# Optimization experiments

Measured on AMD Instinct MI355X. Metric: run time of the kernel, lower is better.

## Reference

```python
import jax, jax.numpy as jnp
import numpy as np

K = 3            # attn_kernels
PAD = K // 2
NORM_SCALE = 1.0
EPS = 1e-4


def _conv(x, w, pad):
    # NCHW conv, stride 1, symmetric padding
    return jax.lax.conv_general_dilated(
        x, w, window_strides=(1, 1), padding=[(pad, pad), (pad, pad)],
        dimension_numbers=('NCHW', 'OIHW', 'NCHW'))


def _unfold(x, k, stride, pad):
    # torch.nn.functional.unfold: returns [B, C*k*k, L], feature order (c, kh, kw),
    # L in row-major patch order.
    if pad:
        x = jnp.pad(x, ((0, 0), (0, 0), (pad, pad), (pad, pad)))
    B, C, H, W = x.shape
    oh = (H - k) // stride + 1
    ow = (W - k) // stride + 1
    cols = []
    for i in range(k):          # small fixed k*k loop (k=3)
        for j in range(k):
            cols.append(x[:, :, i:i + stride * (oh - 1) + 1:stride,
                               j:j + stride * (ow - 1) + 1:stride])
    p = jnp.stack(cols, axis=2)             # [B, C, k*k, oh, ow]
    return p.reshape(B, C * k * k, oh * ow)


def setup_inputs() -> dict:
    key = jax.random.key(0)
    k1, k2, k3, k4 = jax.random.split(key, 4)
    B, Cin, Cout, H, W = 8, 192, 192, 96, 96
    fan = Cin * K * K
    x1 = jax.random.normal(k1, (B, Cin, H, W), jnp.float32)
    x2 = jax.random.normal(k2, (B, Cin, H, W), jnp.float32)
    key_w = jax.random.normal(k3, (Cin, Cin, K, K), jnp.float32) / np.sqrt(fan)
    query_w = jax.random.normal(k4, (Cout, Cin, K, K), jnp.float32) / np.sqrt(fan)
    kernel_momentum = jnp.zeros((), jnp.float32)  # init 0.0 as in module
    return {"x1": x1, "x2": x2, "key_w": key_w, "query_w": query_w,
            "kernel_momentum": kernel_momentum}


def reference(x1, x2, key_w, query_w, kernel_momentum):
    B, Cin, H, W = x1.shape
    Cout = query_w.shape[0]
    fk = K * K

    # key: conv then non-overlapping unfold -> [B, fk, Cin, L]
    kf = _unfold(_conv(x1, key_w, PAD), K, stride=K, pad=0)
    L = kf.shape[-1]
    kf = kf.reshape(B, Cin, fk, L).transpose(0, 2, 1, 3)      # [B, fk, Cin, L]

    # query: conv then non-overlapping unfold -> [B, fk, L, Cout]
    qf = _unfold(_conv(x2, query_w, PAD), K, stride=K, pad=0)
    qf = qf.reshape(B, Cout, fk, L).transpose(0, 2, 3, 1)     # [B, fk, L, Cout]

    # attention kernels: [B, fk, Cin, Cout] -> [B, Cout, Cin*fk]
    attn = jnp.einsum('bkcl,bklo->bkco', kf, qf)
    attn = attn.transpose(0, 3, 2, 1).reshape(B, Cout, Cin * fk)

    # custom global mean/std normalization with momentum (torch std is unbiased)
    m = attn.mean()
    s = jnp.std(attn, ddof=1)
    attn = kernel_momentum * attn + NORM_SCALE * (attn - m) / (s + EPS)

    # apply kernels to dense (stride-1, padded) unfold of x1
    v = _unfold(x1, K, stride=1, pad=PAD)                     # [B, Cin*fk, H*W]
    out = jnp.einsum('bcf,bfl->bcl', attn, v)                 # [B, Cout, H*W]
    return out.reshape(B, Cout, H, W)
```

## Files before the change

### kernel.cpp

```cpp
#include <hip/hip_runtime.h>
#include <math.h>

typedef __attribute__((ext_vector_type(8))) short s16x8;
typedef __attribute__((ext_vector_type(4))) short s16x4;
typedef __attribute__((ext_vector_type(4))) float f32x4;

typedef unsigned int u32;
typedef __attribute__((address_space(3))) u32* lds_u32p;
typedef const __attribute__((address_space(1))) u32* glb_u32p;

namespace {

constexpr int B  = 8;
constexpr int C  = 192;
constexpr int H  = 96;
constexpr int W  = 96;
constexpr int FK = 9;
constexpr int HP = 98;
constexpr int L  = 1024;
constexpr int WCHUNK = FK * 12 * 6;
constexpr int WELEM  = WCHUNK * 512;
constexpr size_t XPAD_ELEMS = (size_t)B * HP * HP * 192;

__device__ inline unsigned short f2b(float f) {
    unsigned int x = __float_as_uint(f);
    x += 0x7fffu + ((x >> 16) & 1u);
    return (unsigned short)(x >> 16);
}

__global__ __launch_bounds__(256) void border_zero(unsigned short* __restrict__ xpad) {
    const int c   = blockIdx.x * 256 + threadIdx.x;
    const int c16 = c % 24;
    const int p_  = c / 24;
    const int pos = p_ % 388;
    const int bt  = p_ / 388;
    int yy, xx;
    if (pos < 98)       { yy = 0;          xx = pos; }
    else if (pos < 196) { yy = 97;         xx = pos - 98; }
    else if (pos < 292) { yy = pos - 195;  xx = 0; }
    else                { yy = pos - 291;  xx = 97; }
    const size_t off = (((size_t)bt * HP + yy) * HP + xx) * 192 + c16 * 8;
    *(s16x8*)(xpad + off) = (s16x8){0, 0, 0, 0, 0, 0, 0, 0};
}

__global__ __launch_bounds__(256) void prep_x(const float* __restrict__ x1,
                                              const float* __restrict__ x2,
                                              unsigned short* __restrict__ xpadT) {
    __shared__ float xs[192][33];
    const int tid = threadIdx.x;
    const int x0  = blockIdx.x * 32;
    const int y   = blockIdx.y;
    const int zz  = blockIdx.z;
    const int b   = zz & 7, t = zz >> 3;
    const float* x = t ? x2 : x1;
    unsigned short* dst = xpadT + (size_t)t * XPAD_ELEMS;
    for (int e = tid; e < 192 * 32; e += 256) {
        const int ci = e >> 5, xx = e & 31;
        xs[ci][xx] = x[(((size_t)b * C + ci) * H + y) * W + x0 + xx];
    }
    __syncthreads();
    for (int e = tid; e < 32 * 192; e += 256) {
        const int pos = e / 192, ci = e - pos * 192;
        dst[(((size_t)(b * HP + y + 1)) * HP + x0 + pos + 1) * 192 + ci] = f2b(xs[ci][pos]);
    }
}

__global__ __launch_bounds__(256) void prep_w(const float* __restrict__ kw,
                                              const float* __restrict__ qw,
                                              unsigned short* __restrict__ kwA,
                                              unsigned short* __restrict__ qwA) {
    int idx = blockIdx.x * 256 + threadIdx.x;
    const float* src = kw;
    unsigned short* dst = kwA;
    if (idx >= WELEM) { idx -= WELEM; src = qw; dst = qwA; }
    const int chunk = idx >> 9, within = idx & 511;
    const int lane = within >> 3, t = within & 7;
    const int kg = lane >> 4, r15 = lane & 15;
    const int cc = chunk % 6, c2 = chunk / 6;
    const int cot = c2 % 12, p = c2 / 12;
    const int co = cot * 16 + r15;
    const int ci = cc * 32 + kg * 8 + t;
    dst[idx] = f2b(src[((size_t)co * C + ci) * FK + p]);
}

template <bool OUTF32, bool PERB, bool DUAL>
__global__ __launch_bounds__(256, 3)
void conv_mfma(const unsigned short* __restrict__ xpadA,
               const unsigned short* __restrict__ xpadB,
               const unsigned short* __restrict__ wA,
               const unsigned short* __restrict__ wB,
               void* __restrict__ youtA,
               void* __restrict__ youtB) {
    __shared__ __align__(16) char smem[2][19200];
    const int tid  = threadIdx.x;
    const int y    = blockIdx.x;
    const int sx   = blockIdx.y;
    const int zz   = blockIdx.z;
    const int b    = DUAL ? (zz & 7) : zz;
    const int t    = DUAL ? (zz >> 3) : 0;
    const unsigned short* xpadT = (DUAL && t) ? xpadB : xpadA;
    const unsigned short* wbase = (DUAL && t) ? wB : wA;
    void* yout = (DUAL && t) ? youtB : youtA;
    const int lane = tid & 63, wc = tid >> 6;
    const int ln15 = lane & 15, kg = lane >> 4;

    const unsigned short* wp = PERB ? (wbase + (size_t)b * WELEM) : wbase;

    int gfull[4];
#pragma unroll
    for (int it = 0; it < 4; ++it) {
        const int m = it * 256 + tid;
        const int q = m / 24, c16 = m - q * 24;
        gfull[it] = (sx * 48 + q) * 384 + ((c16 * 16) ^ ((q & 7) << 4));
    }
    int gtail = 0;
    if (tid < 176) {
        const int m = 1024 + tid;
        const int q = m / 24, c16 = m - q * 24;
        gtail = (sx * 48 + q) * 384 + ((c16 * 16) ^ ((q & 7) << 4));
    }

    auto stage = [&](char* lb, int prow) {
        const char* rowbase = (const char*)(xpadT + ((size_t)(b * HP + prow)) * HP * 192);
#pragma unroll
        for (int it = 0; it < 4; ++it)
            __builtin_amdgcn_global_load_lds(
                (glb_u32p)(const void*)(rowbase + gfull[it]),
                (lds_u32p)(void*)(lb + it * 4096 + wc * 1024), 16, 0, 0);
        if (tid < 176)
            __builtin_amdgcn_global_load_lds(
                (glb_u32p)(const void*)(rowbase + gtail),
                (lds_u32p)(void*)(lb + 16384 + wc * 1024), 16, 0, 0);
    };

    f32x4 acc[3][3];
#pragma unroll
    for (int i = 0; i < 3; ++i)
#pragma unroll
        for (int j = 0; j < 3; ++j)
            acc[i][j] = (f32x4){0.f, 0.f, 0.f, 0.f};

    stage(smem[0], y);

    for (int dy = 0; dy < 3; ++dy) {
        asm volatile("s_waitcnt vmcnt(0)" ::: "memory");
        __syncthreads();
        const char* lb = smem[dy & 1];

#pragma unroll
        for (int cc = 0; cc < 6; ++cc) {
            s16x8 af[3][3];
#pragma unroll
            for (int dx = 0; dx < 3; ++dx)
#pragma unroll
                for (int i = 0; i < 3; ++i) {
                    const int chunkid = ((3 * dy + dx) * 12 + wc * 3 + i) * 6 + cc;
                    af[dx][i] = *(const s16x8*)(wp + (size_t)chunkid * 512 + lane * 8);
                }
            if (cc == 5) {
                __builtin_amdgcn_sched_barrier(0);
                if (dy < 2) stage((char*)smem[(dy + 1) & 1], y + dy + 1);
                __builtin_amdgcn_sched_barrier(0);
            }
            s16x8 bv[3][3];
#pragma unroll
            for (int j = 0; j < 3; ++j)
#pragma unroll
                for (int dx = 0; dx < 3; ++dx) {
                    const int q = j * 16 + ln15 + dx;
                    bv[j][dx] = *(const s16x8*)(lb + q * 384 +
                                    ((cc * 64 + kg * 16) ^ ((q & 7) << 4)));
                }
#pragma unroll
            for (int i = 0; i < 3; ++i)
#pragma unroll
                for (int j = 0; j < 3; ++j)
#pragma unroll
                    for (int dx = 0; dx < 3; ++dx)
                        acc[i][j] = __builtin_amdgcn_mfma_f32_16x16x32_bf16(
                            af[dx][i], bv[j][dx], acc[i][j], 0, 0, 0);
        }
    }

    if (!OUTF32) {
        unsigned short* yb = (unsigned short*)yout;
        const int ph = y % 3, lh = y / 3;
        int poff[3];
#pragma unroll
        for (int j = 0; j < 3; ++j) {
            const int s  = sx * 48 + j * 16 + ln15;
            const int pw = s % 3, lw = s / 3;
            poff[j] = ((b * FK + ph * 3 + pw) * C) * L + lh * 32 + lw;
        }
#pragma unroll
        for (int i = 0; i < 3; ++i)
#pragma unroll
            for (int rr = 0; rr < 4; ++rr) {
                const int co = wc * 48 + i * 16 + kg * 4 + rr;
#pragma unroll
                for (int j = 0; j < 3; ++j)
                    yb[(size_t)poff[j] + co * L] = f2b(acc[i][j][rr]);
            }
    } else {
        float* yf = (float*)yout;
#pragma unroll
        for (int i = 0; i < 3; ++i)
#pragma unroll
            for (int rr = 0; rr < 4; ++rr) {
                const int co = wc * 48 + i * 16 + kg * 4 + rr;
                const size_t base = (((size_t)b * C + co) * H + y) * W;
#pragma unroll
                for (int j = 0; j < 3; ++j)
                    yf[base + sx * 48 + j * 16 + ln15] = acc[i][j][rr];
            }
    }
}

__global__ __launch_bounds__(256, 3)
void attn_mfma(const unsigned short* __restrict__ kcS,
               const unsigned short* __restrict__ qcS,
               float* __restrict__ attnT,
               double* __restrict__ part) {
    __shared__ __align__(16) char smem[2][24576];
    const int tid  = threadIdx.x;
    const int lane = tid & 63, wid = tid >> 6;
    const int wq   = wid & 1, wp = wid >> 1;
    const int ln15 = lane & 15, kg = lane >> 4;
    const int of   = blockIdx.x & 1, cf = blockIdx.x >> 1;
    const int p    = blockIdx.y, b = blockIdx.z;

    const char* Abase = (const char*)(kcS + ((size_t)(b * FK + p) * C + cf * 96) * L);
    const char* Bbase = (const char*)(qcS + ((size_t)(b * FK + p) * C + of * 96) * L);

    int gofs[3];
#pragma unroll
    for (int it = 0; it < 3; ++it) {
        const int chunk = it * 256 + tid;
        const int row = chunk >> 3, c16 = chunk & 7;
        gofs[it] = row * 2048 + ((c16 * 16) ^ ((row & 7) << 4));
    }

    auto stage = [&](int bufi, int t) {
        const char* Ab = Abase + t * 128;
        const char* Bb = Bbase + t * 128;
        char* lb = (char*)smem[bufi];
#pragma unroll
        for (int it = 0; it < 3; ++it)
            __builtin_amdgcn_global_load_lds(
                (glb_u32p)(const void*)(Ab + gofs[it]),
                (lds_u32p)(void*)(lb + it * 4096 + wid * 1024), 16, 0, 0);
#pragma unroll
        for (int it = 0; it < 3; ++it)
            __builtin_amdgcn_global_load_lds(
                (glb_u32p)(const void*)(Bb + gofs[it]),
                (lds_u32p)(void*)(lb + 12288 + it * 4096 + wid * 1024), 16, 0, 0);
    };

    f32x4 acc[3][3];
#pragma unroll
    for (int i = 0; i < 3; ++i)
#pragma unroll
        for (int j = 0; j < 3; ++j)
            acc[i][j] = (f32x4){0.f, 0.f, 0.f, 0.f};

    stage(0, 0);
    asm volatile("s_waitcnt vmcnt(0)" ::: "memory");
    __syncthreads();

    for (int t = 0; t < 16; ++t) {
        if (t < 15) stage((t + 1) & 1, t + 1);
        const char* lb = (const char*)smem[t & 1];
#pragma unroll
        for (int ks = 0; ks < 2; ++ks) {
            s16x8 af[3], bf[3];
#pragma unroll
            for (int i = 0; i < 3; ++i) {
                const int row = wp * 48 + i * 16 + ln15;
                af[i] = *(const s16x8*)(lb + row * 128 +
                                        ((ks * 64 + kg * 16) ^ ((row & 7) << 4)));
            }
#pragma unroll
            for (int j = 0; j < 3; ++j) {
                const int row = wq * 48 + j * 16 + ln15;
                bf[j] = *(const s16x8*)(lb + 12288 + row * 128 +
                                        ((ks * 64 + kg * 16) ^ ((row & 7) << 4)));
            }
#pragma unroll
            for (int i = 0; i < 3; ++i)
#pragma unroll
                for (int j = 0; j < 3; ++j)
                    acc[i][j] = __builtin_amdgcn_mfma_f32_16x16x32_bf16(
                        af[i], bf[j], acc[i][j], 0, 0, 0);
        }
        if (t < 15) {
            asm volatile("s_waitcnt vmcnt(0)" ::: "memory");
            __syncthreads();
        }
    }

    __syncthreads();
    double s = 0.0, ss = 0.0;
#pragma unroll
    for (int i = 0; i < 3; ++i)
#pragma unroll
        for (int j = 0; j < 3; ++j)
#pragma unroll
            for (int r = 0; r < 4; ++r) {
                const double v = (double)acc[i][j][r];
                s += v; ss += v * v;
            }
    double* ls  = (double*)&smem[0][0];
    double* lss = ls + 256;
    ls[tid] = s; lss[tid] = ss;
    __syncthreads();
    for (int st = 128; st; st >>= 1) {
        if (tid < st) { ls[tid] += ls[tid + st]; lss[tid] += lss[tid + st]; }
        __syncthreads();
    }
    if (tid == 0) {
        const int bf_ = ((b * FK + p) << 2) + blockIdx.x;
        part[2 * bf_]     = ls[0];
        part[2 * bf_ + 1] = lss[0];
    }

    float* ap = attnT + (size_t)(b * FK + p) * C * C;
#pragma unroll
    for (int i = 0; i < 3; ++i) {
        const int c0 = cf * 96 + wp * 48 + i * 16 + kg * 4;
#pragma unroll
        for (int j = 0; j < 3; ++j) {
            const int o = of * 96 + wq * 48 + j * 16 + ln15;
            *(f32x4*)(ap + o * C + c0) = acc[i][j];
        }
    }
}

__global__ __launch_bounds__(256) void finalize_k(const double* __restrict__ part,
                                                  const float* __restrict__ momp,
                                                  float* __restrict__ scal) {
    __shared__ double ls[256], lss[256];
    double s = 0.0, ss = 0.0;
    for (int i = threadIdx.x; i < 288; i += 256) {
        s += part[2 * i]; ss += part[2 * i + 1];
    }
    ls[threadIdx.x] = s; lss[threadIdx.x] = ss;
    __syncthreads();
    for (int st = 128; st; st >>= 1) {
        if (threadIdx.x < st) {
            ls[threadIdx.x]  += ls[threadIdx.x + st];
            lss[threadIdx.x] += lss[threadIdx.x + st];
        }
        __syncthreads();
    }
    if (threadIdx.x == 0) {
        const double n    = (double)(B * FK * C * C);
        const double mean = ls[0] / n;
        double var        = (lss[0] - ls[0] * ls[0] / n) / (n - 1.0);
        if (var < 0.0) var = 0.0;
        const double scale = 1.0 / (sqrt(var) + 1e-4);
        scal[0] = (float)((double)momp[0] + scale);
        scal[1] = (float)(-mean * scale);
    }
}

__global__ __launch_bounds__(256) void norm_w(const float* __restrict__ attnT,
                                              const float* __restrict__ scal,
                                              unsigned short* __restrict__ o) {
    const float alpha = scal[0], beta = scal[1];
    const int g = (blockIdx.x * 256 + threadIdx.x) * 4;
    const int chunk = g >> 9, within = g & 511;
    const int lane = within >> 3, t0 = within & 7;
    const int cc = chunk % 6, c2 = chunk / 6;
    const int cot = c2 % 12, pb = c2 / 12;
    const int p = pb % FK, b = pb / FK;
    const int co = cot * 16 + (lane & 15);
    const int ci = cc * 32 + (lane >> 4) * 8 + t0;
    const float4 v = *(const float4*)(attnT + (((size_t)(b * FK + p) * C + co) * C + ci));
    s16x4 r;
    r[0] = (short)f2b(fmaf(alpha, v.x, beta));
    r[1] = (short)f2b(fmaf(alpha, v.y, beta));
    r[2] = (short)f2b(fmaf(alpha, v.z, beta));
    r[3] = (short)f2b(fmaf(alpha, v.w, beta));
    *(s16x4*)(o + g) = r;
}

}

extern "C" void kernel_launch(void* const* d_in, const int* in_sizes, int n_in,
                              void* d_out, int out_size, void* d_ws, size_t ws_size,
                              hipStream_t stream) {
    (void)in_sizes; (void)n_in; (void)out_size; (void)ws_size;
    const float* x1   = (const float*)d_in[0];
    const float* x2   = (const float*)d_in[1];
    const float* kw   = (const float*)d_in[2];
    const float* qw   = (const float*)d_in[3];
    const float* momp = (const float*)d_in[4];

    char* ws = (char*)d_ws;
    unsigned short* xpad1 = (unsigned short*)ws;
    unsigned short* xpad2 = (unsigned short*)(ws + 29503488);
    unsigned short* kwA   = (unsigned short*)(ws + 59006976);
    unsigned short* qwA   = (unsigned short*)(ws + 59670528);
    unsigned short* kcS   = (unsigned short*)(ws + 60334080);
    float*          attnT = (float*)(ws + 88645632);
    double*         part  = (double*)(ws + 99262464);
    float*          scal  = (float*)(ws + 99278848);
    unsigned short* normW = kcS;
    unsigned short* qcS   = (unsigned short*)d_out;

    border_zero<<<582, 256, 0, stream>>>(xpad1);

    prep_x<<<dim3(3, 96, 16), 256, 0, stream>>>(x1, x2, xpad1);
    prep_w<<<2592, 256, 0, stream>>>(kw, qw, kwA, qwA);

    conv_mfma<false, false, true><<<dim3(96, 2, 16), 256, 0, stream>>>(
        xpad1, xpad2, kwA, qwA, kcS, qcS);

    attn_mfma<<<dim3(4, 9, 8), 256, 0, stream>>>(kcS, qcS, attnT, part);
    finalize_k<<<1, 256, 0, stream>>>(part, momp, scal);

    norm_w<<<2592, 256, 0, stream>>>(attnT, scal, normW);
    conv_mfma<true, true, false><<<dim3(96, 2, 8), 256, 0, stream>>>(
        xpad1, nullptr, normW, nullptr, (float*)d_out, nullptr);
}
```

Before: 265.3 us.

## Compute two output rows per conv block to reuse weight fragments

Each conv block now produces two output rows instead of one. It loads all four needed padded input rows into LDS up front, and every weight fragment read from global memory feeds MFMAs for both rows, which halves weight traffic per output. The cost is the loss of the double-buffered staging overlap. LDS use grows to about 77KB and the accumulators double, so launch bounds drop to 2 blocks per SM and the grid is halved.

```diff
diff --git a/kernel.cpp b/kernel.cpp
--- a/kernel.cpp
+++ b/kernel.cpp
@@ -84,16 +84,16 @@
 }
 
 template <bool OUTF32, bool PERB, bool DUAL>
-__global__ __launch_bounds__(256, 3)
+__global__ __launch_bounds__(256, 2)
 void conv_mfma(const unsigned short* __restrict__ xpadA,
                const unsigned short* __restrict__ xpadB,
                const unsigned short* __restrict__ wA,
                const unsigned short* __restrict__ wB,
                void* __restrict__ youtA,
                void* __restrict__ youtB) {
-    __shared__ __align__(16) char smem[2][19200];
+    __shared__ __align__(16) char smem[4 * 50 * 384];
     const int tid  = threadIdx.x;
-    const int y    = blockIdx.x;
+    const int y0   = blockIdx.x * 2;
     const int sx   = blockIdx.y;
     const int zz   = blockIdx.z;
     const int b    = DUAL ? (zz & 7) : zz;
@@ -106,47 +106,37 @@
 
     const unsigned short* wp = PERB ? (wbase + (size_t)b * WELEM) : wbase;
 
-    int gfull[4];
-#pragma unroll
-    for (int it = 0; it < 4; ++it) {
-        const int m = it * 256 + tid;
-        const int q = m / 24, c16 = m - q * 24;
-        gfull[it] = (sx * 48 + q) * 384 + ((c16 * 16) ^ ((q & 7) << 4));
-    }
-    int gtail = 0;
-    if (tid < 176) {
-        const int m = 1024 + tid;
-        const int q = m / 24, c16 = m - q * 24;
-        gtail = (sx * 48 + q) * 384 + ((c16 * 16) ^ ((q & 7) << 4));
-    }
-
-    auto stage = [&](char* lb, int prow) {
-        const char* rowbase = (const char*)(xpadT + ((size_t)(b * HP + prow)) * HP * 192);
-#pragma unroll
-        for (int it = 0; it < 4; ++it)
-            __builtin_amdgcn_global_load_lds(
-                (glb_u32p)(const void*)(rowbase + gfull[it]),
-                (lds_u32p)(void*)(lb + it * 4096 + wc * 1024), 16, 0, 0);
-        if (tid < 176)
-            __builtin_amdgcn_global_load_lds(
-                (glb_u32p)(const void*)(rowbase + gtail),
-                (lds_u32p)(void*)(lb + 16384 + wc * 1024), 16, 0, 0);
-    };
-
-    f32x4 acc[3][3];
-#pragma unroll
-    for (int i = 0; i < 3; ++i)
-#pragma unroll
-        for (int j = 0; j < 3; ++j)
-            acc[i][j] = (f32x4){0.f, 0.f, 0.f, 0.f};
-
-    stage(smem[0], y);
-
+    {
+        const char* base = (const char*)(xpadT + ((size_t)(b * HP + y0)) * HP * 192);
+#pragma unroll
+        for (int it = 0; it < 19; ++it) {
+            const int m = it * 256 + tid;
+            if (it < 18 || tid < 192) {
+                const int r  = m / 1200, rm = m - r * 1200;
+                const int p  = rm / 24,  c16 = rm - p * 24;
+                const int go = r * 37632 + (sx * 48 + p) * 384 +
+                               ((c16 * 16) ^ ((p & 7) << 4));
+                __builtin_amdgcn_global_load_lds(
+                    (glb_u32p)(const void*)(base + go),
+                    (lds_u32p)(void*)(smem + it * 4096 + wc * 1024), 16, 0, 0);
+            }
+        }
+    }
+
+    f32x4 acc[2][3][3];
+#pragma unroll
+    for (int yy = 0; yy < 2; ++yy)
+#pragma unroll
+        for (int i = 0; i < 3; ++i)
+#pragma unroll
+            for (int j = 0; j < 3; ++j)
+                acc[yy][i][j] = (f32x4){0.f, 0.f, 0.f, 0.f};
+
+    asm volatile("s_waitcnt vmcnt(0)" ::: "memory");
+    __syncthreads();
+
+#pragma unroll
     for (int dy = 0; dy < 3; ++dy) {
-        asm volatile("s_waitcnt vmcnt(0)" ::: "memory");
-        __syncthreads();
-        const char* lb = smem[dy & 1];
-
 #pragma unroll
         for (int cc = 0; cc < 6; ++cc) {
             s16x8 af[3][3];
@@ -157,62 +147,65 @@
                     const int chunkid = ((3 * dy + dx) * 12 + wc * 3 + i) * 6 + cc;
                     af[dx][i] = *(const s16x8*)(wp + (size_t)chunkid * 512 + lane * 8);
                 }
-            if (cc == 5) {
-                __builtin_amdgcn_sched_barrier(0);
-                if (dy < 2) stage((char*)smem[(dy + 1) & 1], y + dy + 1);
-                __builtin_amdgcn_sched_barrier(0);
-            }
-            s16x8 bv[3][3];
-#pragma unroll
-            for (int j = 0; j < 3; ++j)
-#pragma unroll
-                for (int dx = 0; dx < 3; ++dx) {
-                    const int q = j * 16 + ln15 + dx;
-                    bv[j][dx] = *(const s16x8*)(lb + q * 384 +
-                                    ((cc * 64 + kg * 16) ^ ((q & 7) << 4)));
+#pragma unroll
+            for (int yy = 0; yy < 2; ++yy) {
+                const int rr = yy + dy;
+                s16x8 bv[3][3];
+#pragma unroll
+                for (int j = 0; j < 3; ++j)
+#pragma unroll
+                    for (int dx = 0; dx < 3; ++dx) {
+                        const int q = j * 16 + ln15 + dx;
+                        bv[j][dx] = *(const s16x8*)(smem + (rr * 50 + q) * 384 +
+                                        ((cc * 64 + kg * 16) ^ ((q & 7) << 4)));
+                    }
+#pragma unroll
+                for (int i = 0; i < 3; ++i)
+#pragma unroll
+                    for (int j = 0; j < 3; ++j)
+#pragma unroll
+                        for (int dx = 0; dx < 3; ++dx)
+                            acc[yy][i][j] = __builtin_amdgcn_mfma_f32_16x16x32_bf16(
+                                af[dx][i], bv[j][dx], acc[yy][i][j], 0, 0, 0);
+            }
+        }
+    }
+
+#pragma unroll
+    for (int yy = 0; yy < 2; ++yy) {
+        const int y = y0 + yy;
+        if (!OUTF32) {
+            unsigned short* yb = (unsigned short*)yout;
+            const int ph = y % 3, lh = y / 3;
+            int poff[3];
+#pragma unroll
+            for (int j = 0; j < 3; ++j) {
+                const int s  = sx * 48 + j * 16 + ln15;
+                const int pw = s % 3, lw = s / 3;
+                poff[j] = ((b * FK + ph * 3 + pw) * C) * L + lh * 32 + lw;
+            }
+#pragma unroll
+            for (int i = 0; i < 3; ++i)
+#pragma unroll
+                for (int rr = 0; rr < 4; ++rr) {
+                    const int co = wc * 48 + i * 16 + kg * 4 + rr;
+#pragma unroll
+                    for (int j = 0; j < 3; ++j)
+                        yb[(size_t)poff[j] + co * L] = f2b(acc[yy][i][j][rr]);
                 }
+        } else {
+            float* yf = (float*)yout;
 #pragma unroll
             for (int i = 0; i < 3; ++i)
 #pragma unroll
-                for (int j = 0; j < 3; ++j)
-#pragma unroll
-                    for (int dx = 0; dx < 3; ++dx)
-                        acc[i][j] = __builtin_amdgcn_mfma_f32_16x16x32_bf16(
-                            af[dx][i], bv[j][dx], acc[i][j], 0, 0, 0);
-        }
-    }
-
-    if (!OUTF32) {
-        unsigned short* yb = (unsigned short*)yout;
-        const int ph = y % 3, lh = y / 3;
-        int poff[3];
-#pragma unroll
-        for (int j = 0; j < 3; ++j) {
-            const int s  = sx * 48 + j * 16 + ln15;
-            const int pw = s % 3, lw = s / 3;
-            poff[j] = ((b * FK + ph * 3 + pw) * C) * L + lh * 32 + lw;
-        }
-#pragma unroll
-        for (int i = 0; i < 3; ++i)
-#pragma unroll
-            for (int rr = 0; rr < 4; ++rr) {
-                const int co = wc * 48 + i * 16 + kg * 4 + rr;
-#pragma unroll
-                for (int j = 0; j < 3; ++j)
-                    yb[(size_t)poff[j] + co * L] = f2b(acc[i][j][rr]);
-            }
-    } else {
-        float* yf = (float*)yout;
-#pragma unroll
-        for (int i = 0; i < 3; ++i)
-#pragma unroll
-            for (int rr = 0; rr < 4; ++rr) {
-                const int co = wc * 48 + i * 16 + kg * 4 + rr;
-                const size_t base = (((size_t)b * C + co) * H + y) * W;
-#pragma unroll
-                for (int j = 0; j < 3; ++j)
-                    yf[base + sx * 48 + j * 16 + ln15] = acc[i][j][rr];
-            }
+                for (int rr = 0; rr < 4; ++rr) {
+                    const int co = wc * 48 + i * 16 + kg * 4 + rr;
+                    const size_t base = (((size_t)b * C + co) * H + y) * W;
+#pragma unroll
+                    for (int j = 0; j < 3; ++j)
+                        yf[base + sx * 48 + j * 16 + ln15] = acc[yy][i][j][rr];
+                }
+        }
     }
 }
 
@@ -413,13 +406,13 @@
     prep_x<<<dim3(3, 96, 16), 256, 0, stream>>>(x1, x2, xpad1);
     prep_w<<<2592, 256, 0, stream>>>(kw, qw, kwA, qwA);
 
-    conv_mfma<false, false, true><<<dim3(96, 2, 16), 256, 0, stream>>>(
+    conv_mfma<false, false, true><<<dim3(48, 2, 16), 256, 0, stream>>>(
         xpad1, xpad2, kwA, qwA, kcS, qcS);
 
     attn_mfma<<<dim3(4, 9, 8), 256, 0, stream>>>(kcS, qcS, attnT, part);
     finalize_k<<<1, 256, 0, stream>>>(part, momp, scal);
 
     norm_w<<<2592, 256, 0, stream>>>(attnT, scal, normW);
-    conv_mfma<true, true, false><<<dim3(96, 2, 8), 256, 0, stream>>>(
+    conv_mfma<true, true, false><<<dim3(48, 2, 8), 256, 0, stream>>>(
         xpad1, nullptr, normW, nullptr, (float*)d_out, nullptr);
 }
```

Result: slower. 556.9 us (+109.9%).

## Widen conv tiles to full output rows and drop LDS double buffering

Applied to the files above, without the earlier changes.

The conv kernel now computes a full 96-pixel output row per block instead of two 48-pixel halves. This halves the grid and reuses each weight fragment load across six column tiles instead of three, cutting redundant weight traffic. The double-buffered LDS staging is replaced by a single full-row buffer loaded after a barrier, so the next row's global-to-LDS load no longer overlaps compute. Fewer blocks, more accumulator registers and no occupancy hint may reduce latency hiding.

```diff
diff --git a/kernel.cpp b/kernel.cpp
--- a/kernel.cpp
+++ b/kernel.cpp
@@ -84,18 +84,17 @@
 }
 
 template <bool OUTF32, bool PERB, bool DUAL>
-__global__ __launch_bounds__(256, 3)
+__global__ __launch_bounds__(256)
 void conv_mfma(const unsigned short* __restrict__ xpadA,
                const unsigned short* __restrict__ xpadB,
                const unsigned short* __restrict__ wA,
                const unsigned short* __restrict__ wB,
                void* __restrict__ youtA,
                void* __restrict__ youtB) {
-    __shared__ __align__(16) char smem[2][19200];
+    __shared__ __align__(16) char smem[HP * 384];
     const int tid  = threadIdx.x;
     const int y    = blockIdx.x;
-    const int sx   = blockIdx.y;
-    const int zz   = blockIdx.z;
+    const int zz   = blockIdx.y;
     const int b    = DUAL ? (zz & 7) : zz;
     const int t    = DUAL ? (zz >> 3) : 0;
     const unsigned short* xpadT = (DUAL && t) ? xpadB : xpadA;
@@ -106,89 +105,79 @@
 
     const unsigned short* wp = PERB ? (wbase + (size_t)b * WELEM) : wbase;
 
-    int gfull[4];
-#pragma unroll
-    for (int it = 0; it < 4; ++it) {
+    int gofs[9];
+#pragma unroll
+    for (int it = 0; it < 9; ++it) {
         const int m = it * 256 + tid;
         const int q = m / 24, c16 = m - q * 24;
-        gfull[it] = (sx * 48 + q) * 384 + ((c16 * 16) ^ ((q & 7) << 4));
+        gofs[it] = q * 384 + ((c16 * 16) ^ ((q & 7) << 4));
     }
     int gtail = 0;
-    if (tid < 176) {
-        const int m = 1024 + tid;
+    if (tid < 48) {
+        const int m = 2304 + tid;
         const int q = m / 24, c16 = m - q * 24;
-        gtail = (sx * 48 + q) * 384 + ((c16 * 16) ^ ((q & 7) << 4));
-    }
-
-    auto stage = [&](char* lb, int prow) {
-        const char* rowbase = (const char*)(xpadT + ((size_t)(b * HP + prow)) * HP * 192);
-#pragma unroll
-        for (int it = 0; it < 4; ++it)
+        gtail = q * 384 + ((c16 * 16) ^ ((q & 7) << 4));
+    }
+
+    auto stage = [&](int prow) {
+        const char* rb = (const char*)(xpadT + ((size_t)(b * HP + prow)) * HP * 192);
+#pragma unroll
+        for (int it = 0; it < 9; ++it)
             __builtin_amdgcn_global_load_lds(
-                (glb_u32p)(const void*)(rowbase + gfull[it]),
-                (lds_u32p)(void*)(lb + it * 4096 + wc * 1024), 16, 0, 0);
-        if (tid < 176)
+                (glb_u32p)(const void*)(rb + gofs[it]),
+                (lds_u32p)(void*)(smem + it * 4096 + wc * 1024), 16, 0, 0);
+        if (tid < 48)
             __builtin_amdgcn_global_load_lds(
-                (glb_u32p)(const void*)(rowbase + gtail),
-                (lds_u32p)(void*)(lb + 16384 + wc * 1024), 16, 0, 0);
+                (glb_u32p)(const void*)(rb + gtail),
+                (lds_u32p)(void*)(smem + 36864 + wc * 1024), 16, 0, 0);
     };
 
-    f32x4 acc[3][3];
+    f32x4 acc[3][6];
 #pragma unroll
     for (int i = 0; i < 3; ++i)
 #pragma unroll
-        for (int j = 0; j < 3; ++j)
+        for (int j = 0; j < 6; ++j)
             acc[i][j] = (f32x4){0.f, 0.f, 0.f, 0.f};
 
-    stage(smem[0], y);
-
+    stage(y);
+
+#pragma unroll 1
     for (int dy = 0; dy < 3; ++dy) {
         asm volatile("s_waitcnt vmcnt(0)" ::: "memory");
         __syncthreads();
-        const char* lb = smem[dy & 1];
-
-#pragma unroll
+
+#pragma unroll 1
         for (int cc = 0; cc < 6; ++cc) {
-            s16x8 af[3][3];
-#pragma unroll
-            for (int dx = 0; dx < 3; ++dx)
-#pragma unroll
-                for (int i = 0; i < 3; ++i) {
-                    const int chunkid = ((3 * dy + dx) * 12 + wc * 3 + i) * 6 + cc;
-                    af[dx][i] = *(const s16x8*)(wp + (size_t)chunkid * 512 + lane * 8);
+#pragma unroll
+            for (int dx = 0; dx < 3; ++dx) {
+                const int cid = (((3 * dy + dx) * 12 + wc * 3) * 6 + cc);
+                const s16x8 af0 = *(const s16x8*)(wp + (size_t)cid * 512 + lane * 8);
+                const s16x8 af1 = *(const s16x8*)(wp + (size_t)(cid + 6) * 512 + lane * 8);
+                const s16x8 af2 = *(const s16x8*)(wp + (size_t)(cid + 12) * 512 + lane * 8);
+#pragma unroll
+                for (int j = 0; j < 6; ++j) {
+                    const int q = j * 16 + ln15 + dx;
+                    const s16x8 bv = *(const s16x8*)(smem + q * 384 +
+                                        ((cc * 64 + kg * 16) ^ ((q & 7) << 4)));
+                    acc[0][j] = __builtin_amdgcn_mfma_f32_16x16x32_bf16(af0, bv, acc[0][j], 0, 0, 0);
+                    acc[1][j] = __builtin_amdgcn_mfma_f32_16x16x32_bf16(af1, bv, acc[1][j], 0, 0, 0);
+                    acc[2][j] = __builtin_amdgcn_mfma_f32_16x16x32_bf16(af2, bv, acc[2][j], 0, 0, 0);
                 }
-            if (cc == 5) {
-                __builtin_amdgcn_sched_barrier(0);
-                if (dy < 2) stage((char*)smem[(dy + 1) & 1], y + dy + 1);
-                __builtin_amdgcn_sched_barrier(0);
-            }
-            s16x8 bv[3][3];
-#pragma unroll
-            for (int j = 0; j < 3; ++j)
-#pragma unroll
-                for (int dx = 0; dx < 3; ++dx) {
-                    const int q = j * 16 + ln15 + dx;
-                    bv[j][dx] = *(const s16x8*)(lb + q * 384 +
-                                    ((cc * 64 + kg * 16) ^ ((q & 7) << 4)));
-                }
-#pragma unroll
-            for (int i = 0; i < 3; ++i)
-#pragma unroll
-                for (int j = 0; j < 3; ++j)
-#pragma unroll
-                    for (int dx = 0; dx < 3; ++dx)
-                        acc[i][j] = __builtin_amdgcn_mfma_f32_16x16x32_bf16(
-                            af[dx][i], bv[j][dx], acc[i][j], 0, 0, 0);
+            }
+        }
+        if (dy < 2) {
+            __syncthreads();
+            stage(y + dy + 1);
         }
     }
 
     if (!OUTF32) {
         unsigned short* yb = (unsigned short*)yout;
         const int ph = y % 3, lh = y / 3;
-        int poff[3];
-#pragma unroll
-        for (int j = 0; j < 3; ++j) {
-            const int s  = sx * 48 + j * 16 + ln15;
+        int poff[6];
+#pragma unroll
+        for (int j = 0; j < 6; ++j) {
+            const int s  = j * 16 + ln15;
             const int pw = s % 3, lw = s / 3;
             poff[j] = ((b * FK + ph * 3 + pw) * C) * L + lh * 32 + lw;
         }
@@ -198,7 +187,7 @@
             for (int rr = 0; rr < 4; ++rr) {
                 const int co = wc * 48 + i * 16 + kg * 4 + rr;
 #pragma unroll
-                for (int j = 0; j < 3; ++j)
+                for (int j = 0; j < 6; ++j)
                     yb[(size_t)poff[j] + co * L] = f2b(acc[i][j][rr]);
             }
     } else {
@@ -210,8 +199,8 @@
                 const int co = wc * 48 + i * 16 + kg * 4 + rr;
                 const size_t base = (((size_t)b * C + co) * H + y) * W;
 #pragma unroll
-                for (int j = 0; j < 3; ++j)
-                    yf[base + sx * 48 + j * 16 + ln15] = acc[i][j][rr];
+                for (int j = 0; j < 6; ++j)
+                    yf[base + j * 16 + ln15] = acc[i][j][rr];
             }
     }
 }
@@ -413,13 +402,13 @@
     prep_x<<<dim3(3, 96, 16), 256, 0, stream>>>(x1, x2, xpad1);
     prep_w<<<2592, 256, 0, stream>>>(kw, qw, kwA, qwA);
 
-    conv_mfma<false, false, true><<<dim3(96, 2, 16), 256, 0, stream>>>(
+    conv_mfma<false, false, true><<<dim3(96, 16), 256, 0, stream>>>(
         xpad1, xpad2, kwA, qwA, kcS, qcS);
 
     attn_mfma<<<dim3(4, 9, 8), 256, 0, stream>>>(kcS, qcS, attnT, part);
     finalize_k<<<1, 256, 0, stream>>>(part, momp, scal);
 
     norm_w<<<2592, 256, 0, stream>>>(attnT, scal, normW);
-    conv_mfma<true, true, false><<<dim3(96, 2, 8), 256, 0, stream>>>(
+    conv_mfma<true, true, false><<<dim3(96, 8), 256, 0, stream>>>(
         xpad1, nullptr, normW, nullptr, (float*)d_out, nullptr);
 }
```

Result: faster. 259.3 us (-2.3%).

## Specialize final conv to full-row tiles with per-wave weight reuse

Applied to the files above, without the earlier changes.

Splits the templated conv into a front kernel for the dual key/query convs and a new final conv kernel. The final conv kernel processes a whole 96-pixel row per block (6 column tiles instead of 3), staging the full padded row in LDS. Each weight fragment is loaded directly from global memory once and reused across six MMA column tiles, which halves weight traffic and redundant halo staging. In exchange it doubles the accumulators, drops the double-buffered LDS pipeline in favour of a single buffer with syncs, and uses a larger LDS footprint that may lower occupancy.

```diff
diff --git a/kernel.cpp b/kernel.cpp
--- a/kernel.cpp
+++ b/kernel.cpp
@@ -83,28 +83,25 @@
     dst[idx] = f2b(src[((size_t)co * C + ci) * FK + p]);
 }
 
-template <bool OUTF32, bool PERB, bool DUAL>
 __global__ __launch_bounds__(256, 3)
-void conv_mfma(const unsigned short* __restrict__ xpadA,
-               const unsigned short* __restrict__ xpadB,
-               const unsigned short* __restrict__ wA,
-               const unsigned short* __restrict__ wB,
-               void* __restrict__ youtA,
-               void* __restrict__ youtB) {
+void conv_front(const unsigned short* __restrict__ xpadA,
+                const unsigned short* __restrict__ xpadB,
+                const unsigned short* __restrict__ wA,
+                const unsigned short* __restrict__ wB,
+                void* __restrict__ youtA,
+                void* __restrict__ youtB) {
     __shared__ __align__(16) char smem[2][19200];
     const int tid  = threadIdx.x;
     const int y    = blockIdx.x;
     const int sx   = blockIdx.y;
     const int zz   = blockIdx.z;
-    const int b    = DUAL ? (zz & 7) : zz;
-    const int t    = DUAL ? (zz >> 3) : 0;
-    const unsigned short* xpadT = (DUAL && t) ? xpadB : xpadA;
-    const unsigned short* wbase = (DUAL && t) ? wB : wA;
-    void* yout = (DUAL && t) ? youtB : youtA;
+    const int b    = zz & 7;
+    const int t    = zz >> 3;
+    const unsigned short* xpadT = t ? xpadB : xpadA;
+    const unsigned short* wp    = t ? wB : wA;
+    void* yout = t ? youtB : youtA;
     const int lane = tid & 63, wc = tid >> 6;
     const int ln15 = lane & 15, kg = lane >> 4;
-
-    const unsigned short* wp = PERB ? (wbase + (size_t)b * WELEM) : wbase;
 
     int gfull[4];
 #pragma unroll
@@ -182,38 +179,115 @@
         }
     }
 
-    if (!OUTF32) {
-        unsigned short* yb = (unsigned short*)yout;
-        const int ph = y % 3, lh = y / 3;
-        int poff[3];
-#pragma unroll
-        for (int j = 0; j < 3; ++j) {
-            const int s  = sx * 48 + j * 16 + ln15;
-            const int pw = s % 3, lw = s / 3;
-            poff[j] = ((b * FK + ph * 3 + pw) * C) * L + lh * 32 + lw;
-        }
-#pragma unroll
-        for (int i = 0; i < 3; ++i)
-#pragma unroll
-            for (int rr = 0; rr < 4; ++rr) {
-                const int co = wc * 48 + i * 16 + kg * 4 + rr;
-#pragma unroll
-                for (int j = 0; j < 3; ++j)
-                    yb[(size_t)poff[j] + co * L] = f2b(acc[i][j][rr]);
+    unsigned short* yb = (unsigned short*)yout;
+    const int ph = y % 3, lh = y / 3;
+    int poff[3];
+#pragma unroll
+    for (int j = 0; j < 3; ++j) {
+        const int s  = sx * 48 + j * 16 + ln15;
+        const int pw = s % 3, lw = s / 3;
+        poff[j] = ((b * FK + ph * 3 + pw) * C) * L + lh * 32 + lw;
+    }
+#pragma unroll
+    for (int i = 0; i < 3; ++i)
+#pragma unroll
+        for (int rr = 0; rr < 4; ++rr) {
+            const int co = wc * 48 + i * 16 + kg * 4 + rr;
+#pragma unroll
+            for (int j = 0; j < 3; ++j)
+                yb[(size_t)poff[j] + co * L] = f2b(acc[i][j][rr]);
+        }
+}
+
+__global__ __launch_bounds__(256)
+void conv_final(const unsigned short* __restrict__ xpadT,
+                const unsigned short* __restrict__ wA,
+                float* __restrict__ yout) {
+    __shared__ __align__(16) char smem[HP * 384];
+    const int tid  = threadIdx.x;
+    const int y    = blockIdx.x;
+    const int b    = blockIdx.y;
+    const int lane = tid & 63, wc = tid >> 6;
+    const int ln15 = lane & 15, kg = lane >> 4;
+
+    const unsigned short* wp = wA + (size_t)b * WELEM;
+
+    int gofs[9];
+#pragma unroll
+    for (int it = 0; it < 9; ++it) {
+        const int m = it * 256 + tid;
+        const int q = m / 24, c16 = m - q * 24;
+        gofs[it] = q * 384 + ((c16 * 16) ^ ((q & 7) << 4));
+    }
+    int gtail = 0;
+    if (tid < 48) {
+        const int m = 2304 + tid;
+        const int q = m / 24, c16 = m - q * 24;
+        gtail = q * 384 + ((c16 * 16) ^ ((q & 7) << 4));
+    }
+
+    auto stage = [&](int prow) {
+        const char* rb = (const char*)(xpadT + ((size_t)(b * HP + prow)) * HP * 192);
+#pragma unroll
+        for (int it = 0; it < 9; ++it)
+            __builtin_amdgcn_global_load_lds(
+                (glb_u32p)(const void*)(rb + gofs[it]),
+                (lds_u32p)(void*)(smem + it * 4096 + wc * 1024), 16, 0, 0);
+        if (tid < 48)
+            __builtin_amdgcn_global_load_lds(
+                (glb_u32p)(const void*)(rb + gtail),
+                (lds_u32p)(void*)(smem + 36864 + wc * 1024), 16, 0, 0);
+    };
+
+    f32x4 acc[3][6];
+#pragma unroll
+    for (int i = 0; i < 3; ++i)
+#pragma unroll
+        for (int j = 0; j < 6; ++j)
+            acc[i][j] = (f32x4){0.f, 0.f, 0.f, 0.f};
+
+    stage(y);
+
+#pragma unroll 1
+    for (int dy = 0; dy < 3; ++dy) {
+        asm volatile("s_waitcnt vmcnt(0)" ::: "memory");
+        __syncthreads();
+
+#pragma unroll 1
+        for (int cc = 0; cc < 6; ++cc) {
+#pragma unroll
+            for (int dx = 0; dx < 3; ++dx) {
+                const int cid = (((3 * dy + dx) * 12 + wc * 3) * 6 + cc);
+                const s16x8 af0 = *(const s16x8*)(wp + (size_t)cid * 512 + lane * 8);
+                const s16x8 af1 = *(const s16x8*)(wp + (size_t)(cid + 6) * 512 + lane * 8);
+                const s16x8 af2 = *(const s16x8*)(wp + (size_t)(cid + 12) * 512 + lane * 8);
+#pragma unroll
+                for (int j = 0; j < 6; ++j) {
+                    const int q = j * 16 + ln15 + dx;
+                    const s16x8 bv = *(const s16x8*)(smem + q * 384 +
+                                        ((cc * 64 + kg * 16) ^ ((q & 7) << 4)));
+                    acc[0][j] = __builtin_amdgcn_mfma_f32_16x16x32_bf16(af0, bv, acc[0][j], 0, 0, 0);
+                    acc[1][j] = __builtin_amdgcn_mfma_f32_16x16x32_bf16(af1, bv, acc[1][j], 0, 0, 0);
+                    acc[2][j] = __builtin_amdgcn_mfma_f32_16x16x32_bf16(af2, bv, acc[2][j], 0, 0, 0);
+                }
             }
-    } else {
-        float* yf = (float*)yout;
-#pragma unroll
-        for (int i = 0; i < 3; ++i)
-#pragma unroll
-            for (int rr = 0; rr < 4; ++rr) {
-                const int co = wc * 48 + i * 16 + kg * 4 + rr;
-                const size_t base = (((size_t)b * C + co) * H + y) * W;
-#pragma unroll
-                for (int j = 0; j < 3; ++j)
-                    yf[base + sx * 48 + j * 16 + ln15] = acc[i][j][rr];
-            }
-    }
+        }
+        if (dy < 2) {
+            __syncthreads();
+            stage(y + dy + 1);
+        }
+    }
+
+#pragma unroll
+    for (int i = 0; i < 3; ++i)
+#pragma unroll
+        for (int rr = 0; rr < 4; ++rr) {
+            const int co = wc * 48 + i * 16 + kg * 4 + rr;
+            const size_t base = (((size_t)b * C + co) * H + y) * W;
+#pragma unroll
+            for (int j = 0; j < 6; ++j)
+                yout[base + j * 16 + ln15] = acc[i][j][rr];
+        }
 }
 
 __global__ __launch_bounds__(256, 3)
@@ -413,13 +487,12 @@
     prep_x<<<dim3(3, 96, 16), 256, 0, stream>>>(x1, x2, xpad1);
     prep_w<<<2592, 256, 0, stream>>>(kw, qw, kwA, qwA);
 
-    conv_mfma<false, false, true><<<dim3(96, 2, 16), 256, 0, stream>>>(
+    conv_front<<<dim3(96, 2, 16), 256, 0, stream>>>(
         xpad1, xpad2, kwA, qwA, kcS, qcS);
 
     attn_mfma<<<dim3(4, 9, 8), 256, 0, stream>>>(kcS, qcS, attnT, part);
     finalize_k<<<1, 256, 0, stream>>>(part, momp, scal);
 
     norm_w<<<2592, 256, 0, stream>>>(attnT, scal, normW);
-    conv_mfma<true, true, false><<<dim3(96, 2, 8), 256, 0, stream>>>(
-        xpad1, nullptr, normW, nullptr, (float*)d_out, nullptr);
-}
+    conv_final<<<dim3(96, 8), 256, 0, stream>>>(xpad1, normW, (float*)d_out);
+}
```

Measured after the change: 248.7 us. 6.3% less time.
